# Kernel tuning notes

Hardware: AMD Instinct MI355X
Metric: run time of the kernel (lower is better)

The kernel has to match this reference:

```python
import jax, jax.numpy as jnp
import numpy as np

N_NODES = 100000
N_EDGES = 1600000
IN_CH = 128
OUT_CH = 128


def setup_inputs() -> dict:
    key = jax.random.key(0)
    k = jax.random.split(key, 6)
    x = jax.random.normal(k[0], (N_NODES, IN_CH), dtype=jnp.float32)
    edge_index = jax.random.randint(k[1], (2, N_EDGES), 0, N_NODES, dtype=jnp.int32)
    # GCNConv linear weights (glorot-ish scale) and biases
    W1 = jax.random.normal(k[2], (IN_CH, OUT_CH), dtype=jnp.float32) / np.sqrt(IN_CH)
    b1 = jnp.zeros((OUT_CH,), dtype=jnp.float32)
    W2 = jax.random.normal(k[3], (OUT_CH, OUT_CH), dtype=jnp.float32) / np.sqrt(OUT_CH)
    b2 = jnp.zeros((OUT_CH,), dtype=jnp.float32)
    return {"x": x, "edge_index": edge_index, "W1": W1, "b1": b1, "W2": W2, "b2": b2}


def gcn_conv(x, src, dst, W, b, n_nodes):
    """PyG GCNConv: add self-loops, symmetric D^-1/2 A D^-1/2 normalization."""
    h = x @ W  # [N, out]
    # degree including the implicit self-loop (weight 1)
    ones = jnp.ones(src.shape[0], dtype=x.dtype)
    deg = jax.ops.segment_sum(ones, dst, num_segments=n_nodes) + 1.0  # [N]
    dinv = jax.lax.rsqrt(deg)  # deg >= 1 so always finite
    coef = dinv[src] * dinv[dst]  # [E] edge norm 1/sqrt(d_i d_j)
    msg = h[src] * coef[:, None]  # [E, out] gather + scale
    agg = jax.ops.segment_sum(msg, dst, num_segments=n_nodes)  # scatter-add
    # self-loop contribution: norm = dinv[i]^2
    agg = agg + h * (dinv * dinv)[:, None]
    return agg + b


def reference(x, edge_index, W1, b1, W2, b2):
    src, dst = edge_index[0], edge_index[1]
    h = jax.nn.relu(gcn_conv(x, src, dst, W1, b1, N_NODES))
    out = jax.nn.relu(gcn_conv(h, src, dst, W2, b2, N_NODES))
    return out
```

## Files before the change

kernel.cpp:

```cpp
#include <hip/hip_runtime.h>


#define NN 100000
#define NBKT 512
#define BKT_W 196
#define CHUNK 8192
#define CAP 6144

typedef __attribute__((ext_vector_type(8))) short bf16x8;
typedef __attribute__((ext_vector_type(4))) float f32x4;

__device__ __forceinline__ ushort f2bf(float f) {
  unsigned u = __float_as_uint(f);
  unsigned r = (u + 0x7fffu + ((u >> 16) & 1u)) >> 16;
  return (ushort)r;
}
__device__ __forceinline__ float bf2f(ushort s) {
  return __uint_as_float(((unsigned)s) << 16);
}
__device__ __forceinline__ unsigned hipair(unsigned ue, unsigned uo) {
  return (uo & 0xffff0000u) | (ue >> 16);
}


__global__ __launch_bounds__(512) void kb_hist(const int* __restrict__ dst,
                                               int* __restrict__ bcnt, int E) {
  __shared__ int h[NBKT];
  for (int i = threadIdx.x; i < NBKT; i += 512) h[i] = 0;
  __syncthreads();
  int base = blockIdx.x * CHUNK;
#pragma unroll 4
  for (int q = 0; q < CHUNK / 512; q++) {
    int e = base + threadIdx.x + q * 512;
    if (e < E) atomicAdd(&h[dst[e] / BKT_W], 1);
  }
  __syncthreads();
  for (int i = threadIdx.x; i < NBKT; i += 512)
    if (h[i]) atomicAdd(&bcnt[i], h[i]);
}

__global__ __launch_bounds__(512) void kb_scan(const int* __restrict__ bcnt,
                                               int* __restrict__ bbase,
                                               int* __restrict__ bcur,
                                               int* __restrict__ row_ptr,
                                               int N, int E) {
  __shared__ int s[NBKT];
  int t = threadIdx.x;
  int v = bcnt[t];
  s[t] = v;
  __syncthreads();
  for (int off = 1; off < NBKT; off <<= 1) {
    int x = (t >= off) ? s[t - off] : 0;
    __syncthreads();
    s[t] += x;
    __syncthreads();
  }
  int ex = s[t] - v;
  bbase[t] = ex;
  bcur[t] = ex;
  if (t == NBKT - 1) bbase[NBKT] = E;
  if (t == 0) row_ptr[N] = E;
}

__global__ __launch_bounds__(512) void kb_scatter(const int* __restrict__ src,
                                                  const int* __restrict__ dst,
                                                  int* __restrict__ bcur,
                                                  int2* __restrict__ pairs, int E) {
  __shared__ int h[NBKT];
  __shared__ int gb[NBKT];
  for (int i = threadIdx.x; i < NBKT; i += 512) h[i] = 0;
  __syncthreads();

  const int base = blockIdx.x * CHUNK;
  const int t = threadIdx.x;
  int rank[CHUNK / 512], bkt[CHUNK / 512], sv[CHUNK / 512], dv[CHUNK / 512];
#pragma unroll
  for (int q = 0; q < CHUNK / 512; q++) {
    int e = base + t + q * 512;
    if (e < E) {
      int d = dst[e];
      int b = d / BKT_W;
      bkt[q] = b;
      sv[q] = src[e];
      dv[q] = d;
      rank[q] = atomicAdd(&h[b], 1);
    } else {
      bkt[q] = -1;
    }
  }
  __syncthreads();
  for (int i = t; i < NBKT; i += 512) {
    int c = h[i];
    gb[i] = c ? atomicAdd(&bcur[i], c) : 0;
  }
  __syncthreads();
#pragma unroll
  for (int q = 0; q < CHUNK / 512; q++) {
    if (bkt[q] >= 0) pairs[(size_t)gb[bkt[q]] + rank[q]] = make_int2(sv[q], dv[q]);
  }
}

__global__ __launch_bounds__(512) void kb_sort(const int* __restrict__ bbase,
                                               const int2* __restrict__ pairs,
                                               int* __restrict__ csr_src,
                                               int* __restrict__ row_ptr,
                                               int N, int E) {
  __shared__ int cnt[256];
  __shared__ int sc[256];
  __shared__ int cur[256];
  __shared__ int stage[CAP];

  const int b = blockIdx.x;
  const int t = threadIdx.x;
  const int lo = bbase[b], hi = bbase[b + 1];
  const int n0 = b * BKT_W;
  int m = hi - lo;
  if (m > CAP) m = CAP;

  if (t < 256) cnt[t] = 0;
  __syncthreads();

  for (int i = t; i < m; i += 512) {
    int2 p = pairs[(size_t)lo + i];
    atomicAdd(&cnt[p.y - n0], 1);
  }
  __syncthreads();

  int v = 0;
  if (t < 256) {
    v = cnt[t];
    sc[t] = v;
  }
  __syncthreads();
  for (int off = 1; off < 256; off <<= 1) {
    int x = 0;
    if (t < 256 && t >= off) x = sc[t - off];
    __syncthreads();
    if (t < 256) sc[t] += x;
    __syncthreads();
  }
  if (t < 256) {
    int ex = sc[t] - v;
    cur[t] = ex;
    int node = n0 + t;
    if (t < BKT_W && node < N) row_ptr[node] = lo + ex;
  }
  __syncthreads();

  for (int i = t; i < m; i += 512) {
    int2 p = pairs[(size_t)lo + i];
    int pos = atomicAdd(&cur[p.y - n0], 1);
    stage[pos] = p.x;
  }
  __syncthreads();

  for (int i = t; i < m; i += 512) csr_src[(size_t)lo + i] = stage[i];
}

__global__ __launch_bounds__(256) void k_dinv(const int* __restrict__ row_ptr,
                                              float* __restrict__ dinv, int N) {
  int i = blockIdx.x * 256 + threadIdx.x;
  if (i < N) dinv[i] = rsqrtf((float)(row_ptr[i + 1] - row_ptr[i]) + 1.0f);
}


__device__ __forceinline__ void cvt_row(const float* __restrict__ p,
                                        bf16x8* hi, bf16x8* lo) {
  float4 v0 = *(const float4*)p;
  float4 v1 = *(const float4*)(p + 4);
  float f[8] = {v0.x, v0.y, v0.z, v0.w, v1.x, v1.y, v1.z, v1.w};
  unsigned hw[4], lw[4];
#pragma unroll
  for (int i = 0; i < 4; ++i) {
    unsigned u0 = __float_as_uint(f[2 * i]);
    unsigned u1 = __float_as_uint(f[2 * i + 1]);
    float l0 = f[2 * i] - __uint_as_float(u0 & 0xffff0000u);
    float l1 = f[2 * i + 1] - __uint_as_float(u1 & 0xffff0000u);
    hw[i] = hipair(u0, u1);
    lw[i] = hipair(__float_as_uint(l0), __float_as_uint(l1));
  }
  uint4 H = make_uint4(hw[0], hw[1], hw[2], hw[3]);
  uint4 L = make_uint4(lw[0], lw[1], lw[2], lw[3]);
  *hi = __builtin_bit_cast(bf16x8, H);
  *lo = __builtin_bit_cast(bf16x8, L);
}

__global__ __launch_bounds__(256) void k_gemm_mfma(const float* __restrict__ X,
                                                   const float* __restrict__ W,
                                                   const float* __restrict__ dinv,
                                                   ushort* __restrict__ hs, int M) {
  __shared__ ushort wt_hi[128 * 128];
  __shared__ ushort wt_lo[128 * 128];

  const int t = threadIdx.x;

  {
    const int n4 = (t & 31) * 4;
    const int kq0 = (t >> 5) * 4;
    for (int it = 0; it < 4; ++it) {
      const int kq = kq0 + it * 32;
      float4 r[4];
#pragma unroll
      for (int j = 0; j < 4; ++j)
        r[j] = *(const float4*)(W + (size_t)(kq + j) * 128 + n4);
#pragma unroll
      for (int q = 0; q < 4; ++q) {
        const int n = n4 + q;
        unsigned u[4], l[4];
#pragma unroll
        for (int j = 0; j < 4; ++j) {
          float f = ((const float*)&r[j])[q];
          u[j] = __float_as_uint(f);
          float lf = f - __uint_as_float(u[j] & 0xffff0000u);
          l[j] = __float_as_uint(lf);
        }
        uint2 hw = make_uint2(hipair(u[0], u[1]), hipair(u[2], u[3]));
        uint2 lw = make_uint2(hipair(l[0], l[1]), hipair(l[2], l[3]));
        const int bo = (n * 256 + kq * 2) ^ ((n & 7) << 4);
        *(uint2*)((char*)wt_hi + bo) = hw;
        *(uint2*)((char*)wt_lo + bo) = lw;
      }
    }
  }
  __syncthreads();

  const int wv = t >> 6;
  const int lane = t & 63;
  const int r0 = blockIdx.x * 128 + wv * 32;
  const int la = lane & 15;
  const int kg = (lane >> 4) * 8;
  const int rowA = min(r0 + la, M - 1);
  const int rowB = min(r0 + 16 + la, M - 1);

  f32x4 acc[2][8];
#pragma unroll
  for (int rs = 0; rs < 2; ++rs)
#pragma unroll
    for (int ct = 0; ct < 8; ++ct) acc[rs][ct] = (f32x4)(0.f);

#pragma unroll
  for (int ks = 0; ks < 4; ++ks) {
    const int koff = ks * 32 + kg;
    bf16x8 ah0, al0, ah1, al1;
    cvt_row(X + (size_t)rowA * 128 + koff, &ah0, &al0);
    cvt_row(X + (size_t)rowB * 128 + koff, &ah1, &al1);
#pragma unroll
    for (int ct = 0; ct < 8; ++ct) {
      const int n = ct * 16 + la;
      const int bo = (n * 256 + koff * 2) ^ ((n & 7) << 4);
      bf16x8 bh = *(const bf16x8*)((const char*)wt_hi + bo);
      bf16x8 bl = *(const bf16x8*)((const char*)wt_lo + bo);
      acc[0][ct] = __builtin_amdgcn_mfma_f32_16x16x32_bf16(ah0, bh, acc[0][ct], 0, 0, 0);
      acc[0][ct] = __builtin_amdgcn_mfma_f32_16x16x32_bf16(ah0, bl, acc[0][ct], 0, 0, 0);
      acc[0][ct] = __builtin_amdgcn_mfma_f32_16x16x32_bf16(al0, bh, acc[0][ct], 0, 0, 0);
      acc[1][ct] = __builtin_amdgcn_mfma_f32_16x16x32_bf16(ah1, bh, acc[1][ct], 0, 0, 0);
      acc[1][ct] = __builtin_amdgcn_mfma_f32_16x16x32_bf16(ah1, bl, acc[1][ct], 0, 0, 0);
      acc[1][ct] = __builtin_amdgcn_mfma_f32_16x16x32_bf16(al1, bh, acc[1][ct], 0, 0, 0);
    }
  }

#pragma unroll
  for (int rs = 0; rs < 2; ++rs) {
#pragma unroll
    for (int j = 0; j < 4; ++j) {
      int r = r0 + rs * 16 + (lane >> 4) * 4 + j;
      if (r < M) {
        float sc = dinv[r];
#pragma unroll
        for (int ct = 0; ct < 8; ++ct)
          hs[(size_t)r * 128 + ct * 16 + la] = f2bf(acc[rs][ct][j] * sc);
      }
    }
  }
}

__global__ __launch_bounds__(256) void k_agg(const int* __restrict__ row_ptr,
                                             const int* __restrict__ csr_src,
                                             const float* __restrict__ dinv,
                                             const ushort* __restrict__ hs,
                                             const float* __restrict__ bias,
                                             float* __restrict__ out, int N) {
  const int node = blockIdx.x * 4 + (threadIdx.x >> 6);
  if (node >= N) return;
  const int lane = threadIdx.x & 63;
  const ushort2* hp = (const ushort2*)hs;

  const int e0 = row_ptr[node];
  const int e1 = row_ptr[node + 1];

  float ax = 0.f, ay = 0.f;
  int e = e0;
  for (; e + 8 <= e1; e += 8) {
    int s[8];
#pragma unroll
    for (int q = 0; q < 8; q++) s[q] = csr_src[e + q];
    ushort2 v[8];
#pragma unroll
    for (int q = 0; q < 8; q++) v[q] = hp[(size_t)s[q] * 64 + lane];
#pragma unroll
    for (int q = 0; q < 8; q++) {
      ax += bf2f(v[q].x);
      ay += bf2f(v[q].y);
    }
  }
  for (; e < e1; ++e) {
    int s = csr_src[e];
    ushort2 v = hp[(size_t)s * 64 + lane];
    ax += bf2f(v.x);
    ay += bf2f(v.y);
  }
  {
    ushort2 v = hp[(size_t)node * 64 + lane];
    ax += bf2f(v.x);
    ay += bf2f(v.y);
  }
  float dv = dinv[node];
  float2 bv = ((const float2*)bias)[lane];
  float2 o;
  o.x = fmaxf(fmaf(ax, dv, bv.x), 0.f);
  o.y = fmaxf(fmaf(ay, dv, bv.y), 0.f);
  ((float2*)out)[(size_t)node * 64 + lane] = o;
}


extern "C" void kernel_launch(void* const* d_in, const int* in_sizes, int n_in,
                              void* d_out, int out_size, void* d_ws, size_t ws_size,
                              hipStream_t stream) {
  const float* x  = (const float*)d_in[0];
  const int*   ei = (const int*)d_in[1];
  const float* W1 = (const float*)d_in[2];
  const float* b1 = (const float*)d_in[3];
  const float* W2 = (const float*)d_in[4];
  const float* b2 = (const float*)d_in[5];
  float* out = (float*)d_out;

  const int N = NN;
  const int E = in_sizes[1] / 2;
  const int* src = ei;
  const int* dst = ei + E;

  char* w = (char*)d_ws;
  auto alloc = [&](size_t bytes) {
    char* p = w;
    w += (bytes + 255) & ~(size_t)255;
    return p;
  };
  float*  dinv    = (float*)alloc((size_t)N * 4);
  int*    row_ptr = (int*)alloc((size_t)(N + 1) * 4);
  int*    bcnt    = (int*)alloc(NBKT * 4);
  int*    bbase   = (int*)alloc((NBKT + 1) * 4);
  int*    bcur    = (int*)alloc(NBKT * 4);
  int*    csr_src = (int*)alloc((size_t)E * 4);
  int2*   pairs   = (int2*)alloc((size_t)E * 8);
  ushort* hs      = (ushort*)alloc((size_t)N * 128 * 2);

  const int EB = (E + CHUNK - 1) / CHUNK;

  hipMemsetAsync(bcnt, 0, NBKT * 4, stream);
  kb_hist<<<EB, 512, 0, stream>>>(dst, bcnt, E);
  kb_scan<<<1, 512, 0, stream>>>(bcnt, bbase, bcur, row_ptr, N, E);
  kb_scatter<<<EB, 512, 0, stream>>>(src, dst, bcur, pairs, E);
  kb_sort<<<NBKT, 512, 0, stream>>>(bbase, pairs, csr_src, row_ptr, N, E);
  k_dinv<<<(N + 255) / 256, 256, 0, stream>>>(row_ptr, dinv, N);

  const int NAGG = (N + 3) / 4;
  const int GB = (N + 127) / 128;

  k_gemm_mfma<<<GB, 256, 0, stream>>>(x, W1, dinv, hs, N);
  k_agg<<<NAGG, 256, 0, stream>>>(row_ptr, csr_src, dinv, hs, b1, out, N);
  k_gemm_mfma<<<GB, 256, 0, stream>>>(out, W2, dinv, hs, N);
  k_agg<<<NAGG, 256, 0, stream>>>(row_ptr, csr_src, dinv, hs, b2, out, N);
}
```

Before: 345.1 us.

## Column-slice feature layout for aggregation and precompute split bf16 weights

The GEMM now writes the bf16 features in a column-sliced layout (8 slices of 16 channels, each contiguous across nodes). The aggregation kernel is split so each block handles one slice for 32 nodes, with 8 lanes per node. The goal is for each slice (about 3.2 MB) to stay cache-resident during the random gathers, at the cost of 8x more index reads and shorter 32-byte gathers. The hi/lo bf16 split and swizzle of the weights also moves into a small one-block kernel, so GEMM blocks only copy preformatted weights into LDS.

```diff
diff --git a/kernel.cpp b/kernel.cpp
--- a/kernel.cpp
+++ b/kernel.cpp
@@ -163,6 +163,28 @@
   if (i < N) dinv[i] = rsqrtf((float)(row_ptr[i + 1] - row_ptr[i]) + 1.0f);
 }
 
+__global__ __launch_bounds__(256) void k_wsplit(const float* __restrict__ W,
+                                                ushort* __restrict__ whi,
+                                                ushort* __restrict__ wlo) {
+  const int t = threadIdx.x;
+#pragma unroll
+  for (int it = 0; it < 16; ++it) {
+    int f4 = it * 256 + t;
+    int k = f4 >> 5;
+    int n4 = (f4 & 31) * 4;
+    float4 v = *(const float4*)(W + (size_t)k * 128 + n4);
+    float f[4] = {v.x, v.y, v.z, v.w};
+#pragma unroll
+    for (int q = 0; q < 4; ++q) {
+      int n = n4 + q;
+      unsigned u = __float_as_uint(f[q]);
+      float lf = f[q] - __uint_as_float(u & 0xffff0000u);
+      int bo = (n * 256 + k * 2) ^ ((n & 7) << 4);
+      *(ushort*)((char*)whi + bo) = (ushort)(u >> 16);
+      *(ushort*)((char*)wlo + bo) = (ushort)(__float_as_uint(lf) >> 16);
+    }
+  }
+}
 
 __device__ __forceinline__ void cvt_row(const float* __restrict__ p,
                                         bf16x8* hi, bf16x8* lo) {
@@ -186,41 +208,19 @@
 }
 
 __global__ __launch_bounds__(256) void k_gemm_mfma(const float* __restrict__ X,
-                                                   const float* __restrict__ W,
+                                                   const ushort* __restrict__ whi,
+                                                   const ushort* __restrict__ wlo,
                                                    const float* __restrict__ dinv,
                                                    ushort* __restrict__ hs, int M) {
   __shared__ ushort wt_hi[128 * 128];
   __shared__ ushort wt_lo[128 * 128];
 
   const int t = threadIdx.x;
-
-  {
-    const int n4 = (t & 31) * 4;
-    const int kq0 = (t >> 5) * 4;
-    for (int it = 0; it < 4; ++it) {
-      const int kq = kq0 + it * 32;
-      float4 r[4];
-#pragma unroll
-      for (int j = 0; j < 4; ++j)
-        r[j] = *(const float4*)(W + (size_t)(kq + j) * 128 + n4);
-#pragma unroll
-      for (int q = 0; q < 4; ++q) {
-        const int n = n4 + q;
-        unsigned u[4], l[4];
-#pragma unroll
-        for (int j = 0; j < 4; ++j) {
-          float f = ((const float*)&r[j])[q];
-          u[j] = __float_as_uint(f);
-          float lf = f - __uint_as_float(u[j] & 0xffff0000u);
-          l[j] = __float_as_uint(lf);
-        }
-        uint2 hw = make_uint2(hipair(u[0], u[1]), hipair(u[2], u[3]));
-        uint2 lw = make_uint2(hipair(l[0], l[1]), hipair(l[2], l[3]));
-        const int bo = (n * 256 + kq * 2) ^ ((n & 7) << 4);
-        *(uint2*)((char*)wt_hi + bo) = hw;
-        *(uint2*)((char*)wt_lo + bo) = lw;
-      }
-    }
+#pragma unroll
+  for (int it = 0; it < 8; ++it) {
+    int o = (it * 256 + t) * 8;
+    *(uint4*)&wt_hi[o] = *(const uint4*)&whi[o];
+    *(uint4*)&wt_lo[o] = *(const uint4*)&wlo[o];
   }
   __syncthreads();
 
@@ -268,58 +268,63 @@
         float sc = dinv[r];
 #pragma unroll
         for (int ct = 0; ct < 8; ++ct)
-          hs[(size_t)r * 128 + ct * 16 + la] = f2bf(acc[rs][ct][j] * sc);
+          hs[(size_t)ct * M * 16 + (size_t)r * 16 + la] = f2bf(acc[rs][ct][j] * sc);
       }
     }
   }
 }
 
-__global__ __launch_bounds__(256) void k_agg(const int* __restrict__ row_ptr,
-                                             const int* __restrict__ csr_src,
-                                             const float* __restrict__ dinv,
-                                             const ushort* __restrict__ hs,
-                                             const float* __restrict__ bias,
-                                             float* __restrict__ out, int N) {
-  const int node = blockIdx.x * 4 + (threadIdx.x >> 6);
+__global__ __launch_bounds__(256) void k_agg8(const int* __restrict__ row_ptr,
+                                              const int* __restrict__ csr_src,
+                                              const float* __restrict__ dinv,
+                                              const ushort* __restrict__ hs,
+                                              const float* __restrict__ bias,
+                                              float* __restrict__ out, int N) {
+  const int cg = blockIdx.x & 7;
+  const int ng = blockIdx.x >> 3;
+  const int wv = threadIdx.x >> 6;
+  const int lane = threadIdx.x & 63;
+  const int sub = lane >> 3;
+  const int cl = lane & 7;
+  const int node = ng * 32 + wv * 8 + sub;
   if (node >= N) return;
-  const int lane = threadIdx.x & 63;
-  const ushort2* hp = (const ushort2*)hs;
+
+  const ushort2* hp = (const ushort2*)(hs + (size_t)cg * N * 16);
 
   const int e0 = row_ptr[node];
   const int e1 = row_ptr[node + 1];
 
   float ax = 0.f, ay = 0.f;
   int e = e0;
-  for (; e + 8 <= e1; e += 8) {
-    int s[8];
-#pragma unroll
-    for (int q = 0; q < 8; q++) s[q] = csr_src[e + q];
-    ushort2 v[8];
-#pragma unroll
-    for (int q = 0; q < 8; q++) v[q] = hp[(size_t)s[q] * 64 + lane];
-#pragma unroll
-    for (int q = 0; q < 8; q++) {
-      ax += bf2f(v[q].x);
-      ay += bf2f(v[q].y);
-    }
+  for (; e + 4 <= e1; e += 4) {
+    int s0 = csr_src[e];
+    int s1 = csr_src[e + 1];
+    int s2 = csr_src[e + 2];
+    int s3 = csr_src[e + 3];
+    ushort2 v0 = hp[(size_t)s0 * 8 + cl];
+    ushort2 v1 = hp[(size_t)s1 * 8 + cl];
+    ushort2 v2 = hp[(size_t)s2 * 8 + cl];
+    ushort2 v3 = hp[(size_t)s3 * 8 + cl];
+    ax += bf2f(v0.x) + bf2f(v1.x) + bf2f(v2.x) + bf2f(v3.x);
+    ay += bf2f(v0.y) + bf2f(v1.y) + bf2f(v2.y) + bf2f(v3.y);
   }
   for (; e < e1; ++e) {
     int s = csr_src[e];
-    ushort2 v = hp[(size_t)s * 64 + lane];
+    ushort2 v = hp[(size_t)s * 8 + cl];
     ax += bf2f(v.x);
     ay += bf2f(v.y);
   }
   {
-    ushort2 v = hp[(size_t)node * 64 + lane];
+    ushort2 v = hp[(size_t)node * 8 + cl];
     ax += bf2f(v.x);
     ay += bf2f(v.y);
   }
   float dv = dinv[node];
-  float2 bv = ((const float2*)bias)[lane];
+  float2 bv = ((const float2*)bias)[cg * 8 + cl];
   float2 o;
   o.x = fmaxf(fmaf(ax, dv, bv.x), 0.f);
   o.y = fmaxf(fmaf(ay, dv, bv.y), 0.f);
-  ((float2*)out)[(size_t)node * 64 + lane] = o;
+  ((float2*)out)[(size_t)node * 64 + cg * 8 + cl] = o;
 }
 
 
@@ -353,6 +358,10 @@
   int*    csr_src = (int*)alloc((size_t)E * 4);
   int2*   pairs   = (int2*)alloc((size_t)E * 8);
   ushort* hs      = (ushort*)alloc((size_t)N * 128 * 2);
+  ushort* w1hi    = (ushort*)alloc(128 * 128 * 2);
+  ushort* w1lo    = (ushort*)alloc(128 * 128 * 2);
+  ushort* w2hi    = (ushort*)alloc(128 * 128 * 2);
+  ushort* w2lo    = (ushort*)alloc(128 * 128 * 2);
 
   const int EB = (E + CHUNK - 1) / CHUNK;
 
@@ -362,12 +371,14 @@
   kb_scatter<<<EB, 512, 0, stream>>>(src, dst, bcur, pairs, E);
   kb_sort<<<NBKT, 512, 0, stream>>>(bbase, pairs, csr_src, row_ptr, N, E);
   k_dinv<<<(N + 255) / 256, 256, 0, stream>>>(row_ptr, dinv, N);
-
-  const int NAGG = (N + 3) / 4;
+  k_wsplit<<<1, 256, 0, stream>>>(W1, w1hi, w1lo);
+  k_wsplit<<<1, 256, 0, stream>>>(W2, w2hi, w2lo);
+
   const int GB = (N + 127) / 128;
-
-  k_gemm_mfma<<<GB, 256, 0, stream>>>(x, W1, dinv, hs, N);
-  k_agg<<<NAGG, 256, 0, stream>>>(row_ptr, csr_src, dinv, hs, b1, out, N);
-  k_gemm_mfma<<<GB, 256, 0, stream>>>(out, W2, dinv, hs, N);
-  k_agg<<<NAGG, 256, 0, stream>>>(row_ptr, csr_src, dinv, hs, b2, out, N);
-}
+  const int AB = ((N + 31) / 32) * 8;
+
+  k_gemm_mfma<<<GB, 256, 0, stream>>>(x, w1hi, w1lo, dinv, hs, N);
+  k_agg8<<<AB, 256, 0, stream>>>(row_ptr, csr_src, dinv, hs, b1, out, N);
+  k_gemm_mfma<<<GB, 256, 0, stream>>>(out, w2hi, w2lo, dinv, hs, N);
+  k_agg8<<<AB, 256, 0, stream>>>(row_ptr, csr_src, dinv, hs, b2, out, N);
+}
```

Measured after the change: 407.4 us. 1.18x slower.
